# Optimization experiments

Hardware: AMD Instinct MI355X
Metric: run time of the kernel (lower is better)

## Reference

```python
import jax, jax.numpy as jnp
import numpy as np

B, V, SX, SY, TIN = 4, 3, 256, 256, 10
WIDTH, M1, M2, STEP, VOUT, NL = 32, 16, 16, 10, 3, 6


def setup_inputs() -> dict:
    key = jax.random.key(0)
    ks = jax.random.split(key, 20)
    n = lambda k, s, sc=1.0: sc * jax.random.normal(k, s, dtype=jnp.float32)
    u = lambda k, s: jax.random.uniform(k, s, dtype=jnp.float32)
    sc = 1.0 / WIDTH
    cshape = (NL, WIDTH, WIDTH, V, M1, M2)
    return {
        'x': n(ks[0], (B, V, SX, SY, TIN)),
        'fc0_w': n(ks[1], (TIN + 2, WIDTH), 0.1), 'fc0_b': jnp.zeros((WIDTH,), jnp.float32),
        'w1r': sc * u(ks[2], cshape), 'w1i': sc * u(ks[3], cshape),
        'w2r': sc * u(ks[4], cshape), 'w2i': sc * u(ks[5], cshape),
        'm1w': n(ks[6], (NL, WIDTH, WIDTH), 0.05), 'm1b': jnp.zeros((NL, WIDTH), jnp.float32),
        'm2w': n(ks[7], (NL, WIDTH, WIDTH), 0.05), 'm2b': jnp.zeros((NL, WIDTH), jnp.float32),
        'ww': n(ks[8], (NL, WIDTH, WIDTH), 0.05), 'wb': jnp.zeros((NL, WIDTH), jnp.float32),
        'bw': n(ks[9], (NL, WIDTH, 2), 0.1), 'bb': jnp.zeros((NL, WIDTH), jnp.float32),
        'fc1v_w': n(ks[10], (V, VOUT), 0.3), 'fc1v_b': jnp.zeros((VOUT,), jnp.float32),
        'fc1t_w': n(ks[11], (WIDTH, 256), 0.05), 'fc1t_b': jnp.zeros((256,), jnp.float32),
        'fc2t_w': n(ks[12], (256, STEP), 0.05), 'fc2t_b': jnp.zeros((STEP,), jnp.float32),
    }


def _gelu(t):
    return jax.nn.gelu(t, approximate=False)  # torch F.gelu default = exact erf


def _conv1x1(x, w, b):
    # 1x1x1 Conv3d: channel mix only. x: (b,c,v,x,y), w: (out,in)
    return jnp.einsum('bcvxy,oc->bovxy', x, w) + b[None, :, None, None, None]


def _spectral(x, w1, w2):
    # x: (b,c,v,X,Y); rfft2 over (X,Y); mode-truncated complex mix, zero-pad, irfft2
    sx, sy = x.shape[-2], x.shape[-1]
    xf = jnp.fft.rfft2(x)  # (b,c,v,X,Y//2+1) complex64
    o1 = jnp.einsum('bivxy,iovxy->bovxy', xf[..., :M1, :M2], w1)
    o2 = jnp.einsum('bivxy,iovxy->bovxy', xf[..., -M1:, :M2], w2)
    out = jnp.zeros((x.shape[0], w1.shape[1]) + xf.shape[2:], jnp.complex64)
    out = out.at[..., :M1, :M2].set(o1).at[..., -M1:, :M2].set(o2)
    return jnp.fft.irfft2(out, s=(sx, sy))


def reference(x, fc0_w, fc0_b, w1r, w1i, w2r, w2i, m1w, m1b, m2w, m2b, ww, wb, bw, bb,
              fc1v_w, fc1v_b, fc1t_w, fc1t_b, fc2t_w, fc2t_b):
    b, v, sx, sy, _ = x.shape
    gx = jnp.broadcast_to(jnp.linspace(0.0, 1.0, sx, dtype=jnp.float32)[:, None], (sx, sy))
    gy = jnp.broadcast_to(jnp.linspace(0.0, 1.0, sy, dtype=jnp.float32)[None, :], (sx, sy))
    grid = jnp.broadcast_to(jnp.stack([gx, gy], -1)[None, None], (b, v, sx, sy, 2))
    h = jnp.concatenate([x, grid], -1) @ fc0_w + fc0_b  # (b,v,X,Y,C)
    h = h.transpose(0, 4, 1, 2, 3)  # (b,C,v,X,Y)
    g = grid.transpose(0, 4, 1, 2, 3)  # (b,2,v,X,Y)

    def layer(i, t):
        x1 = _spectral(t, w1r[i] + 1j * w1i[i], w2r[i] + 1j * w2i[i])
        x1 = _conv1x1(_gelu(_conv1x1(x1, m1w[i], m1b[i])), m2w[i], m2b[i])
        x2 = _conv1x1(t, ww[i], wb[i])
        x3 = _conv1x1(g, bw[i], bb[i])
        return _gelu(x1 + x2 + x3)

    h0 = layer(0, h)
    h = layer(1, h0)
    h = layer(2, h) + h0
    h1 = layer(3, h)
    h = layer(4, h1)
    h = layer(5, h) + h1

    h = h.transpose(0, 1, 3, 4, 2)  # (b,C,X,Y,v)
    h = _gelu(h @ fc1v_w + fc1v_b)
    h = h.transpose(0, 4, 2, 3, 1)  # (b,vout,X,Y,C)
    h = _gelu(h @ fc1t_w + fc1t_b)
    return h @ fc2t_w + fc2t_b  # (b,vout,X,Y,step)
```

## Files before the change

### kernel.cpp

```cpp
#include <hip/hip_runtime.h>
#include <math.h>


#define OFF_A   0
#define OFF_B   25165824
#define OFF_T   50331648
#define OFF_XF  53477376
#define OFF_T1  54263808
#define OFF_T2T 54272000
#define OFF_TAC 54288384
#define OFF_TAS 54296576
#define OFF_TB  54304768

__device__ __forceinline__ float geluf(float x) {
    float a = fabsf(x) * 0.70710678118654752f;
    float t = 1.0f / fmaf(0.3275911f, a, 1.0f);
    float p = t * fmaf(t, fmaf(t, fmaf(t, fmaf(t, 1.061405429f, -1.453152027f),
                                       1.421413741f), -0.284496736f), 0.254829592f);
    float e = __expf(-a * a);
    float erfa = fmaf(-p, e, 1.0f);
    float er = copysignf(erfa, x);
    return 0.5f * x * (1.0f + er);
}

__global__ void k_init_tables(float* __restrict__ ws) {
    const float W0 = 6.2831853071795864769f / 256.0f;
    int stride = gridDim.x * blockDim.x;
    int tid = blockIdx.x * blockDim.x + threadIdx.x;
    for (int i = tid; i < 4096; i += stride) {
        int m = i >> 5, q = i & 31, g = q >> 2, j = q & 3;
        int k0 = 4 * (g & 3) + (g >> 2);
        int k = k0 + 2 * (j >> 1);
        float th = W0 * (float)((k * m) & 255);
        ws[OFF_T1 + i] = (j & 1) ? -sinf(th) : cosf(th);
    }
    for (int idx = tid; idx < 8192; idx += stride) {
        int n = idx >> 5, kx = idx & 31;
        int KX = (kx < 16) ? kx : (kx + 224);
        float th = W0 * (float)((KX * n) & 255);
        ws[OFF_T2T + 2*idx]     = cosf(th);
        ws[OFF_T2T + 2*idx + 1] = sinf(th);
    }
    for (int idx = tid; idx < 8192; idx += stride) {
        int kx = idx >> 8, n = idx & 255;
        int KX = (kx < 16) ? kx : (kx + 224);
        float th = W0 * (float)((KX * n) & 255);
        ws[OFF_TAC + idx] = cosf(th);
        ws[OFF_TAS + idx] = sinf(th);
    }
    for (int idx = tid; idx < 8192; idx += stride) {
        int j = idx >> 8, m = idx & 255, k = j >> 1;
        float th = W0 * (float)((k * m) & 255);
        float beta = (k == 0) ? (1.0f/65536.0f) : (2.0f/65536.0f);
        float val;
        if (j & 1) val = (k == 0) ? 0.0f : -beta * sinf(th);
        else       val = beta * cosf(th);
        ws[OFF_TB + idx] = val;
    }
}

__device__ __forceinline__ void fold_lds(float* lds, int tid) {
#pragma unroll
    for (int it = 0; it < 16; ++it) {
        int pi = it * 256 + tid;
        int r = pi >> 7, mm = pi & 127;
        float* row = lds + r * 257;
        float a = row[mm], c = row[mm + 128];
        row[mm] = a + c; row[mm + 128] = a - c;
    }
}

__device__ __forceinline__ void dft_row_phase(const float* lds, const float* __restrict__ tabF,
                                              float* __restrict__ T, int b, int v, int n, int tid) {
    int r = tid >> 3, g = tid & 7;
    int p = g >> 2, idx = g & 3;
    const float* dp = lds + r * 257 + p * 128;
    const float* tp = tabF + g * 4;
    float a0 = 0.f, a1 = 0.f, a2 = 0.f, a3 = 0.f;
#pragma unroll 4
    for (int m = 0; m < 128; ++m) {
        float d = dp[m];
        float4 t = *(const float4*)(tp + m * 32);
        a0 += d * t.x; a1 += d * t.y; a2 += d * t.z; a3 += d * t.w;
    }
    size_t trow = ((size_t)((b * 32 + r) * 3 + v) * 256 + n) * 32;
    float2 w0; w0.x = a0; w0.y = a1;
    float2 w1; w1.x = a2; w1.y = a3;
    *(float2*)(T + trow + 8 * idx + 2 * p) = w0;
    *(float2*)(T + trow + 8 * idx + 2 * p + 4) = w1;
}

__global__ __launch_bounds__(256) void k_fc0(const float* __restrict__ x,
                                             const float* __restrict__ w,
                                             const float* __restrict__ bias,
                                             float* __restrict__ outA,
                                             float* __restrict__ T,
                                             const float* __restrict__ tabF) {
    __shared__ float lds[32 * 257];
    int blk = blockIdx.x;
    int m = threadIdx.x;
    int n = blk & 255;
    int bv = blk >> 8;
    int v = bv % 3, b = bv / 3;
    const float* xp = x + ((size_t)blk * 256 + m) * 10;
    float xin[10];
#pragma unroll
    for (int t = 0; t < 10; t++) xin[t] = xp[t];
    float gx = (float)n * (1.0f/255.0f), gy = (float)m * (1.0f/255.0f);
    float* op = outA + ((size_t)(b*96) + v) * 65536 + n * 256 + m;
#pragma unroll
    for (int c = 0; c < 32; c++) {
        float a = bias[c] + gx * w[10*32 + c] + gy * w[11*32 + c];
#pragma unroll
        for (int t = 0; t < 10; t++) a += xin[t] * w[t*32 + c];
        op[(size_t)c * 196608] = a;
        lds[c * 257 + m] = a;
    }
    __syncthreads();
    fold_lds(lds, m);
    __syncthreads();
    dft_row_phase(lds, tabF, T, b, v, n, m);
}

__global__ __launch_bounds__(256) void k_dft_x(const float* __restrict__ T,
                                               float* __restrict__ XFp,
                                               const float* __restrict__ tab2) {
    __shared__ float lds[4096];
    int idx = blockIdx.x;
    int half = idx & 1; int blk = idx >> 1;
    int i = blk & 31; int bv = blk >> 5;
    int b = bv / 3, v = bv - 3*b;
    int tid = threadIdx.x;
    const float4* slab = (const float4*)(T + (size_t)((b*32 + i)*3 + v) * 8192 + half * 4096);
#pragma unroll
    for (int j = 0; j < 4; ++j)
        ((float4*)lds)[j * 256 + tid] = slab[j * 256 + tid];
    __syncthreads();
    int ky = tid & 15, kxh = tid >> 4;
    const float* t2b = tab2 + half * 128 * 64;
    float r0=0.f, i0=0.f, r1=0.f, i1=0.f;
#pragma unroll 2
    for (int nn = 0; nn < 128; nn++) {
        float2 t = *(const float2*)(lds + nn * 32 + 2 * ky);
        float2 cs0 = *(const float2*)(t2b + nn*64 + kxh*2);
        float2 cs1 = *(const float2*)(t2b + nn*64 + (kxh+16)*2);
        r0 += t.x*cs0.x + t.y*cs0.y;  i0 += t.y*cs0.x - t.x*cs0.y;
        r1 += t.x*cs1.x + t.y*cs1.y;  i1 += t.y*cs1.x - t.x*cs1.y;
    }
    float2* xfp = (float2*)(XFp + (size_t)(half * 384 + blk) * 1024);
    float2 v0; v0.x = r0; v0.y = i0;
    float2 v1; v1.x = r1; v1.y = i1;
    xfp[kxh*16 + ky] = v0;
    xfp[(kxh+16)*16 + ky] = v1;
}

__global__ __launch_bounds__(256) void k_mixidft(const float* __restrict__ XFp,
                                                 float* __restrict__ T2,
                                                 const float* __restrict__ w1r,
                                                 const float* __restrict__ w1i,
                                                 const float* __restrict__ w2r,
                                                 const float* __restrict__ w2i,
                                                 const float* __restrict__ tac,
                                                 const float* __restrict__ tas, int l) {
    __shared__ float Olds[2048];
    int idx = blockIdx.x;
    int half = idx & 1; int blk = idx >> 1;
    int o = blk & 31; int bv = blk >> 5;
    int b = bv / 3, v = bv - 3*b;
    int tid = threadIdx.x;
    {
        int ky = tid & 15, kxh = tid >> 4;
        float R0=0.f, I0=0.f, R1=0.f, I1=0.f;
#pragma unroll
        for (int i = 0; i < 32; i++) {
            const float2* xa = (const float2*)(XFp + (size_t)(bv*32 + i) * 1024);
            const float2* xb = (const float2*)(XFp + (size_t)(384 + bv*32 + i) * 1024);
            float2 p0 = xa[kxh*16 + ky], q0 = xb[kxh*16 + ky];
            float2 p1 = xa[(kxh+16)*16 + ky], q1 = xb[(kxh+16)*16 + ky];
            float2 xf0; xf0.x = p0.x + q0.x; xf0.y = p0.y + q0.y;
            float2 xf1; xf1.x = p1.x + q1.x; xf1.y = p1.y + q1.y;
            size_t wbase = ((size_t)((l*32 + i)*32 + o)*3 + v) * 256;
            float a1r = w1r[wbase + tid], a1i = w1i[wbase + tid];
            float a2r = w2r[wbase + tid], a2i = w2i[wbase + tid];
            R0 += xf0.x*a1r - xf0.y*a1i;  I0 += xf0.x*a1i + xf0.y*a1r;
            R1 += xf1.x*a2r - xf1.y*a2i;  I1 += xf1.x*a2i + xf1.y*a2r;
        }
        float2 v0; v0.x = R0; v0.y = I0;
        float2 v1; v1.x = R1; v1.y = I1;
        ((float2*)Olds)[kxh*16 + ky] = v0;
        ((float2*)Olds)[(kxh+16)*16 + ky] = v1;
    }
    __syncthreads();
    {
        int ky2 = tid & 31, n8 = tid >> 5;
        int ky = ky2 >> 1, ri = ky2 & 1;
        float* t2p = T2 + (size_t)((b*32 + o)*3 + v) * 8192;
#pragma unroll 2
        for (int ii = 0; ii < 16; ++ii) {
            int n = half * 128 + ii*8 + n8;
            float acc = 0.f;
#pragma unroll
            for (int kx = 0; kx < 32; ++kx) {
                float2 ov = ((const float2*)Olds)[kx*16 + ky];
                float c = tac[kx*256 + n], s = tas[kx*256 + n];
                float ca = ri ? s : c;
                float cb = ri ? c : -s;
                acc += ov.x*ca + ov.y*cb;
            }
            t2p[n*32 + ky2] = acc;
        }
    }
}

template<int HAS_SKIP, int DO_DFT>
__global__ __launch_bounds__(256) void k_conv(
    const float* IN, float* OUT, const float* SK,
    const float* __restrict__ T2, const float* __restrict__ tabB,
    const float* __restrict__ m1w, const float* __restrict__ m1b,
    const float* __restrict__ m2w, const float* __restrict__ m2b,
    const float* __restrict__ ww,  const float* __restrict__ wb,
    const float* __restrict__ bw,  const float* __restrict__ bb,
    float* __restrict__ Tout, const float* __restrict__ tabF, int l)
{
    __shared__ float lds[DO_DFT ? 32 * 257 : 1];
    int blk = blockIdx.x;
    int m = threadIdx.x;
    int n = blk & 255; int bv = blk >> 8;
    int b = bv / 3, v = bv - 3*b;

    float tb[32];
#pragma unroll
    for (int j = 0; j < 32; j++) tb[j] = tabB[j*256 + m];
    const float* t2p = T2 + (size_t)(b*96 + v) * 8192 + n * 32;
    float x1[32];
#pragma unroll
    for (int c = 0; c < 32; c++) {
        const float* tp = t2p + c * 24576;
        float a = 0.f;
#pragma unroll
        for (int j = 0; j < 32; j++) a = fmaf(tp[j], tb[j], a);
        x1[c] = a;
    }

    const float* inp = IN + (size_t)(b*96 + v) * 65536 + n * 256 + m;
    float hv[32];
#pragma unroll
    for (int c = 0; c < 32; c++) hv[c] = inp[(size_t)c * 196608];

    const float* m1wl = m1w + l*1024; const float* m1bl = m1b + l*32;
    float g1[32];
#pragma unroll
    for (int o = 0; o < 32; o++) {
        float a = m1bl[o];
#pragma unroll
        for (int c = 0; c < 32; c++) a = fmaf(m1wl[o*32 + c], x1[c], a);
        g1[o] = geluf(a);
    }

    const float* m2wl = m2w + l*1024; const float* m2bl = m2b + l*32;
    const float* wwl  = ww  + l*1024; const float* wbl  = wb  + l*32;
    const float* bwl  = bw  + l*64;   const float* bbl  = bb  + l*32;
    float gx = (float)n * (1.0f/255.0f), gy = (float)m * (1.0f/255.0f);
    float* outp = OUT + (size_t)(b*96 + v) * 65536 + n * 256 + m;
    const float* skp = SK + (size_t)(b*96 + v) * 65536 + n * 256 + m;

#pragma unroll
    for (int o = 0; o < 32; o++) {
        float a = m2bl[o] + wbl[o] + bbl[o] + bwl[o*2]*gx + bwl[o*2+1]*gy;
#pragma unroll
        for (int c = 0; c < 32; c++) a = fmaf(m2wl[o*32 + c], g1[c], a);
#pragma unroll
        for (int c = 0; c < 32; c++) a = fmaf(wwl[o*32 + c], hv[c], a);
        float val = geluf(a);
        if (HAS_SKIP) val += skp[(size_t)o * 196608];
        outp[(size_t)o * 196608] = val;
        if (DO_DFT) lds[o * 257 + m] = val;
    }
    if (DO_DFT) {
        __syncthreads();
        fold_lds(lds, m);
        __syncthreads();
        dft_row_phase(lds, tabF, Tout, b, v, n, m);
    }
}

__global__ __launch_bounds__(256) void k_final(
    const float* __restrict__ IN, float* __restrict__ OUT,
    const float* __restrict__ w1v, const float* __restrict__ b1v,
    const float* __restrict__ w1t, const float* __restrict__ b1t,
    const float* __restrict__ w2t, const float* __restrict__ b2t)
{
    int blk = blockIdx.x;
    int m = threadIdx.x;
    int vo = blk % 3; int rest = blk / 3;
    int n = rest & 255, b = rest >> 8;
    const float* inp = IN + (size_t)(b*96) * 65536 + n * 256 + m;

    float wv0 = w1v[vo], wv1 = w1v[3 + vo], wv2 = w1v[6 + vo], bv0 = b1v[vo];
    float Av[32];
#pragma unroll
    for (int c = 0; c < 32; c++) {
        float f0 = inp[(size_t)(c*3 + 0) * 65536];
        float f1 = inp[(size_t)(c*3 + 1) * 65536];
        float f2 = inp[(size_t)(c*3 + 2) * 65536];
        Av[c] = geluf(f0*wv0 + f1*wv1 + f2*wv2 + bv0);
    }

    float acc[10];
#pragma unroll
    for (int s = 0; s < 10; s++) acc[s] = 0.f;

#pragma unroll 4
    for (int u = 0; u < 256; u++) {
        float t = b1t[u];
#pragma unroll
        for (int c = 0; c < 32; c++) t = fmaf(Av[c], w1t[c*256 + u], t);
        t = geluf(t);
#pragma unroll
        for (int s = 0; s < 10; s++) acc[s] = fmaf(t, w2t[u*10 + s], acc[s]);
    }

    float* outp = OUT + ((size_t)(b*3 + vo) * 65536 + (size_t)(n * 256 + m)) * 10;
#pragma unroll
    for (int s = 0; s < 10; s++) outp[s] = acc[s] + b2t[s];
}

extern "C" void kernel_launch(void* const* d_in, const int* in_sizes, int n_in,
                              void* d_out, int out_size, void* d_ws, size_t ws_size,
                              hipStream_t stream) {
    const float* x    = (const float*)d_in[0];
    const float* fc0w = (const float*)d_in[1];
    const float* fc0b = (const float*)d_in[2];
    const float* w1r  = (const float*)d_in[3];
    const float* w1i  = (const float*)d_in[4];
    const float* w2r  = (const float*)d_in[5];
    const float* w2i  = (const float*)d_in[6];
    const float* m1w  = (const float*)d_in[7];
    const float* m1b  = (const float*)d_in[8];
    const float* m2w  = (const float*)d_in[9];
    const float* m2b  = (const float*)d_in[10];
    const float* ww   = (const float*)d_in[11];
    const float* wb   = (const float*)d_in[12];
    const float* bw   = (const float*)d_in[13];
    const float* bb   = (const float*)d_in[14];
    const float* w1v  = (const float*)d_in[15];
    const float* b1v  = (const float*)d_in[16];
    const float* w1t  = (const float*)d_in[17];
    const float* b1t  = (const float*)d_in[18];
    const float* w2t  = (const float*)d_in[19];
    const float* b2t  = (const float*)d_in[20];

    float* ws   = (float*)d_ws;
    float* A    = ws + OFF_A;
    float* Bu   = ws + OFF_B;
    float* T    = ws + OFF_T;
    float* XFp  = ws + OFF_XF;
    float* tabF = ws + OFF_T1;
    float* tab2 = ws + OFF_T2T;
    float* tac  = ws + OFF_TAC;
    float* tas  = ws + OFF_TAS;
    float* tbB  = ws + OFF_TB;

    k_init_tables<<<64, 256, 0, stream>>>(ws);
    k_fc0<<<3072, 256, 0, stream>>>(x, fc0w, fc0b, A, T, tabF);

    float* lin [6] = {A, A, Bu, Bu, A, Bu};
    float* lout[6] = {A, Bu, Bu, A, Bu, Bu};
    const float* lskip[6] = {nullptr, nullptr, A, nullptr, nullptr, A};

    for (int l = 0; l < 6; l++) {
        k_dft_x<<<768, 256, 0, stream>>>(T, XFp, tab2);
        k_mixidft<<<768, 256, 0, stream>>>(XFp, T, w1r, w1i, w2r, w2i, tac, tas, l);
        int skip = lskip[l] != nullptr, dodft = (l < 5);
        if (skip && dodft)
            k_conv<1,1><<<3072, 256, 0, stream>>>(lin[l], lout[l], lskip[l], T, tbB,
                                                  m1w, m1b, m2w, m2b, ww, wb, bw, bb, T, tabF, l);
        else if (!skip && dodft)
            k_conv<0,1><<<3072, 256, 0, stream>>>(lin[l], lout[l], nullptr, T, tbB,
                                                  m1w, m1b, m2w, m2b, ww, wb, bw, bb, T, tabF, l);
        else if (skip && !dodft)
            k_conv<1,0><<<3072, 256, 0, stream>>>(lin[l], lout[l], lskip[l], T, tbB,
                                                  m1w, m1b, m2w, m2b, ww, wb, bw, bb, T, tabF, l);
        else
            k_conv<0,0><<<3072, 256, 0, stream>>>(lin[l], lout[l], nullptr, T, tbB,
                                                  m1w, m1b, m2w, m2b, ww, wb, bw, bb, T, tabF, l);
    }

    k_final<<<3072, 256, 0, stream>>>(Bu, (float*)d_out, w1v, b1v, w1t, b1t, w2t, b2t);
}
```

Baseline: 2.542 ms.

## Fold mlp1 channel mix into spectral weights to skip per-pixel matmul

A new pre-pass kernel multiplies the first MLP 1x1 conv weights into the complex spectral mixing weights for every layer. The per-pixel channel mix therefore disappears from the conv kernel, and the inverse-DFT output feeds gelu directly. This is valid because the spectral mix, the inverse DFT and the 1x1 conv are all linear in the channel dimension. It costs an extra weight-folding pass plus about 75 MB of extra workspace, and falls back to the old path when the workspace is too small. Gelu also switches to a hardware reciprocal approximation.

```diff
diff --git a/kernel.cpp b/kernel.cpp
--- a/kernel.cpp
+++ b/kernel.cpp
@@ -11,10 +11,13 @@
 #define OFF_TAC 54288384
 #define OFF_TAS 54296576
 #define OFF_TB  54304768
+#define OFF_FW  54312960
+#define FWSZ    4718592
+#define WS_NEED_FOLD ((size_t)(OFF_FW + 4*FWSZ) * 4)
 
 __device__ __forceinline__ float geluf(float x) {
     float a = fabsf(x) * 0.70710678118654752f;
-    float t = 1.0f / fmaf(0.3275911f, a, 1.0f);
+    float t = __builtin_amdgcn_rcpf(fmaf(0.3275911f, a, 1.0f));
     float p = t * fmaf(t, fmaf(t, fmaf(t, fmaf(t, 1.061405429f, -1.453152027f),
                                        1.421413741f), -0.284496736f), 0.254829592f);
     float e = __expf(-a * a);
@@ -56,6 +59,33 @@
         if (j & 1) val = (k == 0) ? 0.0f : -beta * sinf(th);
         else       val = beta * cosf(th);
         ws[OFF_TB + idx] = val;
+    }
+}
+
+__global__ __launch_bounds__(256) void k_foldw(const float* __restrict__ w1r,
+                                               const float* __restrict__ w1i,
+                                               const float* __restrict__ w2r,
+                                               const float* __restrict__ w2i,
+                                               const float* __restrict__ m1w,
+                                               float* __restrict__ f1r, float* __restrict__ f1i,
+                                               float* __restrict__ f2r, float* __restrict__ f2i) {
+    int blk = blockIdx.x;
+    int p = threadIdx.x;
+    int op = blk & 31; int li = blk >> 5;
+    int l = li >> 5;
+    const float* mrow = m1w + l*1024 + op*32;
+#pragma unroll
+    for (int v = 0; v < 3; ++v) {
+        float a1r = 0.f, a1i = 0.f, a2r = 0.f, a2i = 0.f;
+#pragma unroll 4
+        for (int o = 0; o < 32; ++o) {
+            float mw = mrow[o];
+            size_t idx = ((size_t)(li*32 + o)*3 + v)*256 + p;
+            a1r = fmaf(mw, w1r[idx], a1r); a1i = fmaf(mw, w1i[idx], a1i);
+            a2r = fmaf(mw, w2r[idx], a2r); a2i = fmaf(mw, w2i[idx], a2i);
+        }
+        size_t oidx = ((size_t)(li*32 + op)*3 + v)*256 + p;
+        f1r[oidx] = a1r; f1i[oidx] = a1i; f2r[oidx] = a2r; f2i[oidx] = a2i;
     }
 }
 
@@ -212,7 +242,7 @@
     }
 }
 
-template<int HAS_SKIP, int DO_DFT>
+template<int HAS_SKIP, int DO_DFT, int FOLDED>
 __global__ __launch_bounds__(256) void k_conv(
     const float* IN, float* OUT, const float* SK,
     const float* __restrict__ T2, const float* __restrict__ tabB,
@@ -232,30 +262,41 @@
 #pragma unroll
     for (int j = 0; j < 32; j++) tb[j] = tabB[j*256 + m];
     const float* t2p = T2 + (size_t)(b*96 + v) * 8192 + n * 32;
-    float x1[32];
-#pragma unroll
-    for (int c = 0; c < 32; c++) {
-        const float* tp = t2p + c * 24576;
-        float a = 0.f;
-#pragma unroll
-        for (int j = 0; j < 32; j++) a = fmaf(tp[j], tb[j], a);
-        x1[c] = a;
+    const float* m1bl = m1b + l*32;
+    float g1[32];
+    if (FOLDED) {
+#pragma unroll
+        for (int o = 0; o < 32; o++) {
+            const float* tp = t2p + o * 24576;
+            float a = m1bl[o];
+#pragma unroll
+            for (int j = 0; j < 32; j++) a = fmaf(tp[j], tb[j], a);
+            g1[o] = geluf(a);
+        }
+    } else {
+        float x1[32];
+#pragma unroll
+        for (int c = 0; c < 32; c++) {
+            const float* tp = t2p + c * 24576;
+            float a = 0.f;
+#pragma unroll
+            for (int j = 0; j < 32; j++) a = fmaf(tp[j], tb[j], a);
+            x1[c] = a;
+        }
+        const float* m1wl = m1w + l*1024;
+#pragma unroll
+        for (int o = 0; o < 32; o++) {
+            float a = m1bl[o];
+#pragma unroll
+            for (int c = 0; c < 32; c++) a = fmaf(m1wl[o*32 + c], x1[c], a);
+            g1[o] = geluf(a);
+        }
     }
 
     const float* inp = IN + (size_t)(b*96 + v) * 65536 + n * 256 + m;
     float hv[32];
 #pragma unroll
     for (int c = 0; c < 32; c++) hv[c] = inp[(size_t)c * 196608];
-
-    const float* m1wl = m1w + l*1024; const float* m1bl = m1b + l*32;
-    float g1[32];
-#pragma unroll
-    for (int o = 0; o < 32; o++) {
-        float a = m1bl[o];
-#pragma unroll
-        for (int c = 0; c < 32; c++) a = fmaf(m1wl[o*32 + c], x1[c], a);
-        g1[o] = geluf(a);
-    }
 
     const float* m2wl = m2w + l*1024; const float* m2bl = m2b + l*32;
     const float* wwl  = ww  + l*1024; const float* wbl  = wb  + l*32;
@@ -361,8 +402,19 @@
     float* tas  = ws + OFF_TAS;
     float* tbB  = ws + OFF_TB;
 
+    const bool fold = ws_size >= WS_NEED_FOLD;
+    float* f1r = ws + OFF_FW;
+    float* f1i = ws + OFF_FW + FWSZ;
+    float* f2r = ws + OFF_FW + 2*FWSZ;
+    float* f2i = ws + OFF_FW + 3*FWSZ;
+
     k_init_tables<<<64, 256, 0, stream>>>(ws);
+    if (fold)
+        k_foldw<<<6144, 256, 0, stream>>>(w1r, w1i, w2r, w2i, m1w, f1r, f1i, f2r, f2i);
     k_fc0<<<3072, 256, 0, stream>>>(x, fc0w, fc0b, A, T, tabF);
+
+    const float* u1r = fold ? f1r : w1r;  const float* u1i = fold ? f1i : w1i;
+    const float* u2r = fold ? f2r : w2r;  const float* u2i = fold ? f2i : w2i;
 
     float* lin [6] = {A, A, Bu, Bu, A, Bu};
     float* lout[6] = {A, Bu, Bu, A, Bu, Bu};
@@ -370,20 +422,35 @@
 
     for (int l = 0; l < 6; l++) {
         k_dft_x<<<768, 256, 0, stream>>>(T, XFp, tab2);
-        k_mixidft<<<768, 256, 0, stream>>>(XFp, T, w1r, w1i, w2r, w2i, tac, tas, l);
+        k_mixidft<<<768, 256, 0, stream>>>(XFp, T, u1r, u1i, u2r, u2i, tac, tas, l);
         int skip = lskip[l] != nullptr, dodft = (l < 5);
-        if (skip && dodft)
-            k_conv<1,1><<<3072, 256, 0, stream>>>(lin[l], lout[l], lskip[l], T, tbB,
-                                                  m1w, m1b, m2w, m2b, ww, wb, bw, bb, T, tabF, l);
-        else if (!skip && dodft)
-            k_conv<0,1><<<3072, 256, 0, stream>>>(lin[l], lout[l], nullptr, T, tbB,
-                                                  m1w, m1b, m2w, m2b, ww, wb, bw, bb, T, tabF, l);
-        else if (skip && !dodft)
-            k_conv<1,0><<<3072, 256, 0, stream>>>(lin[l], lout[l], lskip[l], T, tbB,
-                                                  m1w, m1b, m2w, m2b, ww, wb, bw, bb, T, tabF, l);
-        else
-            k_conv<0,0><<<3072, 256, 0, stream>>>(lin[l], lout[l], nullptr, T, tbB,
-                                                  m1w, m1b, m2w, m2b, ww, wb, bw, bb, T, tabF, l);
+        if (fold) {
+            if (skip && dodft)
+                k_conv<1,1,1><<<3072, 256, 0, stream>>>(lin[l], lout[l], lskip[l], T, tbB,
+                                                        m1w, m1b, m2w, m2b, ww, wb, bw, bb, T, tabF, l);
+            else if (!skip && dodft)
+                k_conv<0,1,1><<<3072, 256, 0, stream>>>(lin[l], lout[l], nullptr, T, tbB,
+                                                        m1w, m1b, m2w, m2b, ww, wb, bw, bb, T, tabF, l);
+            else if (skip && !dodft)
+                k_conv<1,0,1><<<3072, 256, 0, stream>>>(lin[l], lout[l], lskip[l], T, tbB,
+                                                        m1w, m1b, m2w, m2b, ww, wb, bw, bb, T, tabF, l);
+            else
+                k_conv<0,0,1><<<3072, 256, 0, stream>>>(lin[l], lout[l], nullptr, T, tbB,
+                                                        m1w, m1b, m2w, m2b, ww, wb, bw, bb, T, tabF, l);
+        } else {
+            if (skip && dodft)
+                k_conv<1,1,0><<<3072, 256, 0, stream>>>(lin[l], lout[l], lskip[l], T, tbB,
+                                                        m1w, m1b, m2w, m2b, ww, wb, bw, bb, T, tabF, l);
+            else if (!skip && dodft)
+                k_conv<0,1,0><<<3072, 256, 0, stream>>>(lin[l], lout[l], nullptr, T, tbB,
+                                                        m1w, m1b, m2w, m2b, ww, wb, bw, bb, T, tabF, l);
+            else if (skip && !dodft)
+                k_conv<1,0,0><<<3072, 256, 0, stream>>>(lin[l], lout[l], lskip[l], T, tbB,
+                                                        m1w, m1b, m2w, m2b, ww, wb, bw, bb, T, tabF, l);
+            else
+                k_conv<0,0,0><<<3072, 256, 0, stream>>>(lin[l], lout[l], nullptr, T, tbB,
+                                                        m1w, m1b, m2w, m2b, ww, wb, bw, bb, T, tabF, l);
+        }
     }
 
     k_final<<<3072, 256, 0, stream>>>(Bu, (float*)d_out, w1v, b1v, w1t, b1t, w2t, b2t);
```

After: 2.464 ms. -3.1%, faster.
